# Performance work log

Hardware: AMD Instinct MI355X
Metric: run time of the kernel (lower is better)

Reference implementation:

```python
import jax, jax.numpy as jnp
import numpy as np
from jax import lax

B, T, N, H, NC = 2, 8, 512, 64, 10
NEG = -1e9
LN_EPS = 1e-5


def _gatv2(x, mask, Wl, Wr, att, b):
    # GATv2Conv (PyG semantics, eval mode): e_ij = att . leaky_relu(Wr x_i + Wl x_j),
    # softmax over source nodes j with self-loops, out_i = sum_j alpha_ij * (Wl x_j).
    # x: (B, N, Fin); mask: (N, N) bool adjacency incl. self-loops; att: (heads, C).
    heads, C = att.shape
    Bn, Nn, _ = x.shape
    xl = (x @ Wl).reshape(Bn, Nn, heads, C)  # source transform
    xr = (x @ Wr).reshape(Bn, Nn, heads, C)  # target transform
    s = jax.nn.leaky_relu(xr[:, :, None] + xl[:, None, :], 0.2)  # (B, Ni, Nj, h, C)
    e = jnp.einsum('bijhc,hc->bijh', s, att)
    e = jnp.where(mask[None, :, :, None], e, NEG)
    alpha = jax.nn.softmax(e, axis=2)  # softmax over neighbors j
    out = jnp.einsum('bijh,bjhc->bihc', alpha, xl)
    return out.reshape(Bn, Nn, heads * C) + b


def _gru_layer(x, Wih, Whh, bih, bhh):
    # torch nn.GRU single layer, batch_first; x: (B, T, Hin)
    h0 = jnp.zeros((x.shape[0], Whh.shape[0]), x.dtype)
    def step(h, xt):
        gi = xt @ Wih + bih
        gh = h @ Whh + bhh
        ir, iz, inn = jnp.split(gi, 3, axis=-1)
        hr, hz, hn = jnp.split(gh, 3, axis=-1)
        r = jax.nn.sigmoid(ir + hr)
        z = jax.nn.sigmoid(iz + hz)
        n = jnp.tanh(inn + r * hn)
        hnew = (1.0 - z) * n + z * h
        return hnew, hnew
    _, ys = lax.scan(step, h0, jnp.swapaxes(x, 0, 1))
    return jnp.swapaxes(ys, 0, 1)


def setup_inputs() -> dict:
    key = jax.random.key(0)
    ks = jax.random.split(key, 20)
    def rn(i, shape, s=0.1):
        return jax.random.normal(ks[i], shape, jnp.float32) * s
    x_seq = jax.random.normal(ks[0], (B, T, N, 1), jnp.float32)
    a = jax.random.uniform(ks[1], (N, N))
    up = jnp.triu((a > 0.95).astype(jnp.float32), 1)
    static_adj = up + up.T  # sparse symmetric 0/1 static graph
    dyn_W = jax.random.normal(ks[2], (N, N), jnp.float32)
    reg_lambda = jnp.array([0.05], jnp.float32)
    return {
        'x_seq': x_seq, 'static_adj': static_adj, 'dyn_W': dyn_W, 'reg_lambda': reg_lambda,
        'g1_Wl': rn(3, (1, H)), 'g1_Wr': rn(4, (1, H)), 'g1_att': rn(5, (4, H // 4)), 'g1_b': jnp.zeros(H),
        'g2_Wl': rn(6, (H, H)), 'g2_Wr': rn(7, (H, H)), 'g2_att': rn(8, (1, H)), 'g2_b': jnp.zeros(H),
        'gru_Wih0': rn(9, (H, 3 * H)), 'gru_Whh0': rn(10, (H, 3 * H)), 'gru_bih0': jnp.zeros(3 * H), 'gru_bhh0': jnp.zeros(3 * H),
        'gru_Wih1': rn(11, (H, 3 * H)), 'gru_Whh1': rn(12, (H, 3 * H)), 'gru_bih1': jnp.zeros(3 * H), 'gru_bhh1': jnp.zeros(3 * H),
        'attn_W': rn(13, (H, 1)), 'attn_b': jnp.zeros(1),
        'cls_W1': rn(14, (H, H)), 'cls_b1': jnp.zeros(H), 'ln_g': jnp.ones(H), 'ln_b': jnp.zeros(H),
        'cls_W2': rn(15, (H, NC)), 'cls_b2': jnp.zeros(NC),
    }


def reference(x_seq, static_adj, dyn_W, reg_lambda,
              g1_Wl, g1_Wr, g1_att, g1_b, g2_Wl, g2_Wr, g2_att, g2_b,
              gru_Wih0, gru_Whh0, gru_bih0, gru_bhh0,
              gru_Wih1, gru_Whh1, gru_bih1, gru_bhh1,
              attn_W, attn_b, cls_W1, cls_b1, ln_g, ln_b, cls_W2, cls_b2):
    Bn, Tn, Nn, _ = x_seq.shape
    lam = jnp.maximum(reg_lambda[0], 0.01)
    t = jnp.arange(Tn, dtype=x_seq.dtype)
    gts = jnp.exp(-lam * t)  # gating values per timestep
    dyn = jax.nn.relu(dyn_W + dyn_W.T)
    fused = gts[:, None, None] * static_adj + (1.0 - gts)[:, None, None] * dyn  # (T, N, N)
    masks = (fused > 0) | jnp.eye(Nn, dtype=bool)[None]  # edge set + self-loops

    def step(carry, inp):
        xt, mask = inp  # xt: (B, N, 1)
        h = jax.nn.elu(_gatv2(xt, mask, g1_Wl, g1_Wr, g1_att, g1_b))
        h = jax.nn.elu(_gatv2(h, mask, g2_Wl, g2_Wr, g2_att, g2_b))
        return carry, h.mean(axis=1)  # (B, H) graph readout

    _, reps = lax.scan(step, 0.0, (jnp.swapaxes(x_seq, 0, 1), masks))
    h_seq = jnp.swapaxes(reps, 0, 1)  # (B, T, H)

    gru_out = _gru_layer(h_seq, gru_Wih0, gru_Whh0, gru_bih0, gru_bhh0)
    gru_out = _gru_layer(gru_out, gru_Wih1, gru_Whh1, gru_bih1, gru_bhh1)

    att_scores = jax.nn.softmax((gru_out @ attn_W + attn_b)[..., 0], axis=1)  # (B, T)
    final = jnp.einsum('bt,bth->bh', att_scores, gru_out)

    z = final @ cls_W1 + cls_b1
    mu = jnp.mean(z, axis=-1, keepdims=True)
    var = jnp.var(z, axis=-1, keepdims=True)
    z = (z - mu) / jnp.sqrt(var + LN_EPS) * ln_g + ln_b
    z = jax.nn.gelu(z, approximate=False)
    logits = z @ cls_W2 + cls_b2
    return logits, gts, att_scores
```

## Files before the change

kernel.cpp:

```cpp
#include <hip/hip_runtime.h>
#include <math.h>

#define BB 2
#define TT 8
#define NN 512
#define HH 64
#define NC 10

typedef unsigned char uchar;

__device__ __forceinline__ float elu1(float v){ return v > 0.f ? v : expm1f(v); }
__device__ __forceinline__ float sigm(float v){ return 1.f/(1.f+expf(-v)); }

__global__ __launch_bounds__(256) void k_mask(
    const float* __restrict__ dW, const float* __restrict__ sadj,
    uchar* __restrict__ M0, uchar* __restrict__ M1,
    float* __restrict__ hseq,
    const float* __restrict__ att1, const float* __restrict__ Wr1,
    const float* __restrict__ Wl1, float* __restrict__ AB,
    const float* __restrict__ Whh0, const float* __restrict__ Wih1,
    const float* __restrict__ Whh1, float4* __restrict__ WT4)
{
    __shared__ float tr[64][65];
    int bx = blockIdx.x, by = blockIdx.y;
    int tid = threadIdx.x;
    if (blockIdx.z == 1){
        int idx = (by*8 + bx)*256 + tid;
        if (idx < 3*4096){
            int m = idx >> 12, r = idx & 4095;
            int gg = r >> 6, k = r & 63;
            const float* W = (m == 0) ? Whh0 : (m == 1) ? Wih1 : Whh1;
            float4 o;
            o.x = W[k*192 + gg];
            o.y = W[k*192 + 64 + gg];
            o.z = W[k*192 + 128 + gg];
            o.w = 0.f;
            WT4[(size_t)m*4096 + r] = o;
        }
        return;
    }
    int i0 = by*64, j0 = bx*64;
    #pragma unroll
    for (int q = 0; q < 4; ++q){
        int r = (tid >> 4) + 16*q, c4 = tid & 15;
        float4 v = *(const float4*)&dW[(size_t)(j0+r)*NN + i0 + 4*c4];
        tr[r][4*c4+0] = v.x; tr[r][4*c4+1] = v.y;
        tr[r][4*c4+2] = v.z; tr[r][4*c4+3] = v.w;
    }
    __syncthreads();
    #pragma unroll
    for (int q = 0; q < 4; ++q){
        int row = (tid >> 4) + 16*q, c4 = tid & 15;
        int i = i0 + row, j = j0 + 4*c4;
        float4 d  = *(const float4*)&dW[(size_t)i*NN + j];
        float4 sa = *(const float4*)&sadj[(size_t)i*NN + j];
        uchar4 m0, m1;
        float dd0 = d.x + tr[4*c4+0][row];
        float dd1 = d.y + tr[4*c4+1][row];
        float dd2 = d.z + tr[4*c4+2][row];
        float dd3 = d.w + tr[4*c4+3][row];
        m0.x = (sa.x > 0.f) || (i == j+0);
        m0.y = (sa.y > 0.f) || (i == j+1);
        m0.z = (sa.z > 0.f) || (i == j+2);
        m0.w = (sa.w > 0.f) || (i == j+3);
        m1.x = m0.x || (dd0 > 0.f);
        m1.y = m0.y || (dd1 > 0.f);
        m1.z = m0.z || (dd2 > 0.f);
        m1.w = m0.w || (dd3 > 0.f);
        *(uchar4*)&M0[(size_t)i*NN + j] = m0;
        *(uchar4*)&M1[(size_t)i*NN + j] = m1;
    }
    int flat = (by*8 + bx)*256 + tid;
    if (flat < BB*TT*HH) hseq[flat] = 0.f;
    if (bx == 0 && by == 0 && tid < 8){
        int h = tid & 3;
        const float* W = (tid < 4) ? Wr1 : Wl1;
        float s = 0.f;
        for (int c = 0; c < 16; ++c) s += att1[h*16+c]*W[h*16+c];
        AB[tid] = s;
    }
}

__global__ __launch_bounds__(256) void k_gat1f(
    const float* __restrict__ x_seq, const uchar* __restrict__ M0,
    const uchar* __restrict__ M1,
    const float* __restrict__ Wl, const float* __restrict__ Wr,
    const float* __restrict__ att, const float* __restrict__ bias,
    const float* __restrict__ AB,
    const float* __restrict__ Wl2, const float* __restrict__ Wr2,
    const float* __restrict__ att2,
    float* __restrict__ xl2, float* __restrict__ xr2,
    float* __restrict__ ui, float* __restrict__ vj)
{
    __shared__ float x_s[NN];
    __shared__ float S_s[4][4];
    __shared__ float h_s[4][HH];
    __shared__ float Wl2_s[64*64];
    __shared__ float Wr2_s[64*64];
    int bt = blockIdx.y; int t = bt % TT;
    int i0 = blockIdx.x * 4;
    int tid = threadIdx.x;
    int il = tid >> 6, jl = tid & 63;
    int i = i0 + il;
    const uchar* M = t ? M1 : M0;
    ((float2*)x_s)[tid] = ((const float2*)(x_seq + bt*NN))[tid];
    #pragma unroll
    for (int q = 0; q < 4; ++q){
        int idx = q*256 + tid;
        ((float4*)Wl2_s)[idx] = ((const float4*)Wl2)[idx];
        ((float4*)Wr2_s)[idx] = ((const float4*)Wr2)[idx];
    }
    __syncthreads();
    float xi = x_s[i];
    const uchar* Mrow = M + (size_t)i*NN;
    float xj[8], msk[8];
    #pragma unroll
    for (int jj = 0; jj < 8; ++jj){
        int j = jj*64 + jl;
        xj[jj] = x_s[j];
        msk[jj] = Mrow[j] ? 1.f : 0.f;
    }
    float sw[4] = {0,0,0,0}, swx[4] = {0,0,0,0};
    for (int h = 0; h < 4; ++h){
        float acc[8] = {0,0,0,0,0,0,0,0};
        #pragma unroll
        for (int c = 0; c < 16; ++c){
            int hc = h*16 + c;
            float wl = Wl[hc];
            float q  = 0.4f * att[hc];
            float pr = xi * Wr[hc];
            #pragma unroll
            for (int jj = 0; jj < 8; ++jj){
                float s = fmaf(xj[jj], wl, pr);
                acc[jj] = fmaf(q, fabsf(s), acc[jj]);
            }
        }
        float lin = 0.6f * xi * AB[h];
        float al6 = 0.6f * AB[4+h];
        #pragma unroll
        for (int jj = 0; jj < 8; ++jj){
            float e = acc[jj] + fmaf(al6, xj[jj], lin);
            float w = msk[jj] * __expf(e);
            sw[h] += w;
            swx[h] = fmaf(w, xj[jj], swx[h]);
        }
    }
    #pragma unroll
    for (int off = 32; off; off >>= 1){
        #pragma unroll
        for (int h = 0; h < 4; ++h){
            sw[h]  += __shfl_down(sw[h],  off);
            swx[h] += __shfl_down(swx[h], off);
        }
    }
    if (jl == 0){
        #pragma unroll
        for (int h = 0; h < 4; ++h) S_s[il][h] = swx[h] / sw[h];
    }
    __syncthreads();
    {
        int hc = tid & 63, row = tid >> 6;
        float v = S_s[row][hc >> 4] * Wl[hc] + bias[hc];
        h_s[row][hc] = elu1(v);
    }
    __syncthreads();
    {
        int c = tid & 63, row = tid >> 6;
        float al = 0.f, ar = 0.f;
        #pragma unroll 8
        for (int k = 0; k < 64; ++k){
            float hv = h_s[row][k];
            al = fmaf(hv, Wl2_s[k*64 + c], al);
            ar = fmaf(hv, Wr2_s[k*64 + c], ar);
        }
        size_t ridx = (size_t)(bt*NN + i0 + row);
        xl2[ridx*HH + c] = al;
        xr2[ridx*HH + c] = ar;
        float a2 = att2[c];
        float pu = a2 * ar, pv = a2 * al;
        #pragma unroll
        for (int off = 32; off; off >>= 1){
            pu += __shfl_down(pu, off);
            pv += __shfl_down(pv, off);
        }
        if (c == 0){ ui[ridx] = pu; vj[ridx] = pv; }
    }
}

__global__ __launch_bounds__(512) void k_gat2(
    const float* __restrict__ xl2, const float* __restrict__ xr2,
    const uchar* __restrict__ M0, const uchar* __restrict__ M1,
    const float* __restrict__ att, const float* __restrict__ ui,
    const float* __restrict__ vj, const float* __restrict__ bias,
    float* __restrict__ hseq)
{
    __shared__ float xl_s[256][68];
    __shared__ float wT_s[256][36];
    __shared__ float v_s[256];
    __shared__ float z_s[32];

    int bt = blockIdx.y, t = bt & 7;
    int i0 = blockIdx.x * 32;
    int base = bt * NN;
    int tid = threadIdx.x;
    const uchar* M = t ? M1 : M0;

    int ig = __builtin_amdgcn_readfirstlane(tid >> 6);
    int jg = tid & 63;
    int ln = jg;
    int ig2 = ln >> 3, cg2 = ln & 7;

    const float* xrp0 = xr2 + (size_t)(base + i0 + ig*4 + 0)*HH;
    const float* xrp1 = xr2 + (size_t)(base + i0 + ig*4 + 1)*HH;
    const float* xrp2 = xr2 + (size_t)(base + i0 + ig*4 + 2)*HH;
    const float* xrp3 = xr2 + (size_t)(base + i0 + ig*4 + 3)*HH;
    float u0 = 0.6f*ui[base + i0 + ig*4 + 0];
    float u1 = 0.6f*ui[base + i0 + ig*4 + 1];
    float u2 = 0.6f*ui[base + i0 + ig*4 + 2];
    float u3 = 0.6f*ui[base + i0 + ig*4 + 3];

    float zreg[4] = {0.f,0.f,0.f,0.f};
    float acc[4][8];
    #pragma unroll
    for (int a = 0; a < 4; ++a)
        #pragma unroll
        for (int r = 0; r < 8; ++r) acc[a][r] = 0.f;

    for (int tile = 0; tile < 2; ++tile){
        int j0 = tile * 256;
        __syncthreads();
        #pragma unroll
        for (int q = 0; q < 8; ++q){
            int idx = q*512 + tid;
            int row = idx >> 4, c4 = idx & 15;
            ((float4*)&xl_s[row][0])[c4] = ((const float4*)&xl2[(size_t)(base+j0+row)*HH])[c4];
        }
        if (tid < 256) v_s[tid] = vj[base + j0 + tid];
        __syncthreads();
        float e[4][4];
        #pragma unroll
        for (int jj = 0; jj < 4; ++jj){
            float vv = 0.6f * v_s[jj*64 + jg];
            e[0][jj] = u0 + vv; e[1][jj] = u1 + vv;
            e[2][jj] = u2 + vv; e[3][jj] = u3 + vv;
        }
        #pragma unroll 4
        for (int c4 = 0; c4 < 16; ++c4){
            float4 a4 = *(const float4*)&att[c4*4];
            float qk[4];
            qk[0] = 0.4f*a4.x; qk[1] = 0.4f*a4.y; qk[2] = 0.4f*a4.z; qk[3] = 0.4f*a4.w;
            float rr[4][4];
            *(float4*)rr[0] = *(const float4*)&xrp0[c4*4];
            *(float4*)rr[1] = *(const float4*)&xrp1[c4*4];
            *(float4*)rr[2] = *(const float4*)&xrp2[c4*4];
            *(float4*)rr[3] = *(const float4*)&xrp3[c4*4];
            float xlv[4][4];
            #pragma unroll
            for (int jj = 0; jj < 4; ++jj)
                *(float4*)xlv[jj] = ((const float4*)&xl_s[jj*64+jg][0])[c4];
            #pragma unroll
            for (int jj = 0; jj < 4; ++jj)
                #pragma unroll
                for (int k = 0; k < 4; ++k){
                    float xc = xlv[jj][k];
                    #pragma unroll
                    for (int ii = 0; ii < 4; ++ii)
                        e[ii][jj] = fmaf(qk[k], fabsf(rr[ii][k] + xc), e[ii][jj]);
                }
        }
        #pragma unroll
        for (int jj = 0; jj < 4; ++jj){
            int j = jj*64 + jg;
            const uchar* mp = &M[(size_t)(i0 + ig*4)*NN + j0 + j];
            float w0 = mp[0]      ? __expf(e[0][jj]) : 0.f;
            float w1 = mp[NN]     ? __expf(e[1][jj]) : 0.f;
            float w2 = mp[2*NN]   ? __expf(e[2][jj]) : 0.f;
            float w3 = mp[3*NN]   ? __expf(e[3][jj]) : 0.f;
            zreg[0] += w0; zreg[1] += w1; zreg[2] += w2; zreg[3] += w3;
            float4 wq; wq.x = w0; wq.y = w1; wq.z = w2; wq.w = w3;
            *(float4*)&wT_s[j][ig*4] = wq;
        }
        __syncthreads();
        #pragma unroll 4
        for (int jj = 0; jj < 32; ++jj){
            int j = ig*32 + jj;
            float w4[4], xa[8];
            *(float4*)w4      = *(const float4*)&wT_s[j][ig2*4];
            *(float4*)&xa[0]  = ((const float4*)&xl_s[j][0])[cg2*2+0];
            *(float4*)&xa[4]  = ((const float4*)&xl_s[j][0])[cg2*2+1];
            #pragma unroll
            for (int a = 0; a < 4; ++a)
                #pragma unroll
                for (int r = 0; r < 8; ++r)
                    acc[a][r] = fmaf(w4[a], xa[r], acc[a][r]);
        }
    }
    __syncthreads();
    #pragma unroll
    for (int off = 32; off; off >>= 1){
        #pragma unroll
        for (int ii = 0; ii < 4; ++ii) zreg[ii] += __shfl_down(zreg[ii], off);
    }
    if (jg == 0){
        #pragma unroll
        for (int ii = 0; ii < 4; ++ii) z_s[ig*4+ii] = zreg[ii];
    }
    float* scratch = &xl_s[0][0];
    if (ig > 0){
        #pragma unroll
        for (int a = 0; a < 4; ++a)
            #pragma unroll
            for (int r = 0; r < 8; ++r)
                scratch[(a*8+r)*448 + (ig-1)*64 + ln] = acc[a][r];
    }
    __syncthreads();
    if (ig == 0){
        float pm[8];
        #pragma unroll
        for (int r = 0; r < 8; ++r) pm[r] = 0.f;
        #pragma unroll
        for (int a = 0; a < 4; ++a){
            float rz = 1.f / z_s[ig2*4 + a];
            #pragma unroll
            for (int r = 0; r < 8; ++r){
                float s = acc[a][r];
                #pragma unroll
                for (int w = 0; w < 7; ++w)
                    s += scratch[(a*8+r)*448 + w*64 + ln];
                float h = elu1(s*rz + bias[cg2*8 + r]);
                pm[r] += h;
            }
        }
        #pragma unroll
        for (int off = 32; off >= 8; off >>= 1){
            #pragma unroll
            for (int r = 0; r < 8; ++r) pm[r] += __shfl_down(pm[r], off);
        }
        if (ig2 == 0){
            #pragma unroll
            for (int r = 0; r < 8; ++r)
                atomicAdd(&hseq[bt*HH + cg2*8 + r], pm[r] * (1.f/(float)NN));
        }
    }
}

__global__ __launch_bounds__(512) void k_gru2(
    const float* __restrict__ hseq, const float* __restrict__ Wih0,
    const float* __restrict__ bih0, const float4* __restrict__ WT4,
    const float* __restrict__ bhh0, const float* __restrict__ Wih1,
    const float* __restrict__ bih1, const float* __restrict__ bhh1,
    const float* __restrict__ lamp, const float* __restrict__ attn_W,
    const float* __restrict__ attn_b, const float* __restrict__ W1,
    const float* __restrict__ b1, const float* __restrict__ ln_g,
    const float* __restrict__ ln_b, const float* __restrict__ W2,
    const float* __restrict__ b2, float* __restrict__ out)
{
    __shared__ float gi_s[BB*TT*192];
    __shared__ float hs_s[BB*TT*HH];
    __shared__ float y_s[BB*TT*HH];
    __shared__ float h_lds[BB][HH];
    __shared__ float part_s[BB][2][3][HH];
    __shared__ float sc_s[BB][TT], at_s[BB][TT];
    __shared__ float fin_s[BB][HH], z_s[BB][HH], g_s[BB][HH];
    __shared__ float mu_s[BB], iv_s[BB];
    int tid = threadIdx.x;
    int wave = tid >> 6, lane = tid & 63;
    int gb = wave >> 1, half = wave & 1;
    bool gruw = (wave < 4);

    float4 Wreg[32];
    if (gruw){
        const float4* src = WT4 + (size_t)lane*64 + half*32;
        #pragma unroll
        for (int kk = 0; kk < 32; ++kk) Wreg[kk] = src[kk];
    }
    for (int v = tid; v < BB*TT*HH; v += 512) hs_s[v] = hseq[v];
    if (tid < BB*HH) h_lds[tid >> 6][tid & 63] = 0.f;
    __syncthreads();
    #pragma unroll
    for (int o = 0; o < 6; ++o){
        int idx = o*512 + tid;
        int b = idx / 192, g = idx % 192;
        float a = bih0[g];
        const float* hr = &hs_s[b*HH];
        #pragma unroll 8
        for (int k = 0; k < HH; ++k) a = fmaf(hr[k], Wih0[k*192 + g], a);
        gi_s[idx] = a;
    }
    __syncthreads();
    {
        float bhr = 0.f, bhz = 0.f, bhn = 0.f;
        if (gruw && half == 0){ bhr = bhh0[lane]; bhz = bhh0[64+lane]; bhn = bhh0[128+lane]; }
        for (int t = 0; t < TT; ++t){
            if (gruw){
                float hh[32];
                #pragma unroll
                for (int q = 0; q < 8; ++q)
                    *(float4*)&hh[q*4] = *(const float4*)&h_lds[gb][half*32 + q*4];
                float ar0=0,ar1=0,az0=0,az1=0,an0=0,an1=0;
                #pragma unroll
                for (int kk = 0; kk < 32; kk += 2){
                    ar0 = fmaf(Wreg[kk].x,   hh[kk],   ar0);
                    az0 = fmaf(Wreg[kk].y,   hh[kk],   az0);
                    an0 = fmaf(Wreg[kk].z,   hh[kk],   an0);
                    ar1 = fmaf(Wreg[kk+1].x, hh[kk+1], ar1);
                    az1 = fmaf(Wreg[kk+1].y, hh[kk+1], az1);
                    an1 = fmaf(Wreg[kk+1].z, hh[kk+1], an1);
                }
                part_s[gb][half][0][lane] = ar0 + ar1;
                part_s[gb][half][1][lane] = az0 + az1;
                part_s[gb][half][2][lane] = an0 + an1;
            }
            __syncthreads();
            if (gruw && half == 0){
                float ghr = part_s[gb][0][0][lane] + part_s[gb][1][0][lane] + bhr;
                float ghz = part_s[gb][0][1][lane] + part_s[gb][1][1][lane] + bhz;
                float ghn = part_s[gb][0][2][lane] + part_s[gb][1][2][lane] + bhn;
                const float* gi = &gi_s[(gb*TT + t)*192];
                float r = sigm(gi[lane] + ghr);
                float z = sigm(gi[64+lane] + ghz);
                float n = tanhf(gi[128+lane] + r*ghn);
                float hn = (1.f - z)*n + z*h_lds[gb][lane];
                h_lds[gb][lane] = hn;
                y_s[(gb*TT + t)*HH + lane] = hn;
            }
            __syncthreads();
        }
    }
    if (gruw){
        const float4* src = WT4 + 2*4096 + (size_t)lane*64 + half*32;
        #pragma unroll
        for (int kk = 0; kk < 32; ++kk) Wreg[kk] = src[kk];
    }
    #pragma unroll
    for (int o = 0; o < 6; ++o){
        int idx = o*512 + tid;
        int b = idx / 192, g = idx % 192;
        float a = bih1[g];
        const float* yr = &y_s[b*HH];
        #pragma unroll 8
        for (int k = 0; k < HH; ++k) a = fmaf(yr[k], Wih1[k*192 + g], a);
        gi_s[idx] = a;
    }
    if (tid < BB*HH) h_lds[tid >> 6][tid & 63] = 0.f;
    __syncthreads();
    {
        float bhr = 0.f, bhz = 0.f, bhn = 0.f;
        if (gruw && half == 0){ bhr = bhh1[lane]; bhz = bhh1[64+lane]; bhn = bhh1[128+lane]; }
        for (int t = 0; t < TT; ++t){
            if (gruw){
                float hh[32];
                #pragma unroll
                for (int q = 0; q < 8; ++q)
                    *(float4*)&hh[q*4] = *(const float4*)&h_lds[gb][half*32 + q*4];
                float ar0=0,ar1=0,az0=0,az1=0,an0=0,an1=0;
                #pragma unroll
                for (int kk = 0; kk < 32; kk += 2){
                    ar0 = fmaf(Wreg[kk].x,   hh[kk],   ar0);
                    az0 = fmaf(Wreg[kk].y,   hh[kk],   az0);
                    an0 = fmaf(Wreg[kk].z,   hh[kk],   an0);
                    ar1 = fmaf(Wreg[kk+1].x, hh[kk+1], ar1);
                    az1 = fmaf(Wreg[kk+1].y, hh[kk+1], az1);
                    an1 = fmaf(Wreg[kk+1].z, hh[kk+1], an1);
                }
                part_s[gb][half][0][lane] = ar0 + ar1;
                part_s[gb][half][1][lane] = az0 + az1;
                part_s[gb][half][2][lane] = an0 + an1;
            }
            __syncthreads();
            if (gruw && half == 0){
                float ghr = part_s[gb][0][0][lane] + part_s[gb][1][0][lane] + bhr;
                float ghz = part_s[gb][0][1][lane] + part_s[gb][1][1][lane] + bhz;
                float ghn = part_s[gb][0][2][lane] + part_s[gb][1][2][lane] + bhn;
                const float* gi = &gi_s[(gb*TT + t)*192];
                float r = sigm(gi[lane] + ghr);
                float z = sigm(gi[64+lane] + ghz);
                float n = tanhf(gi[128+lane] + r*ghn);
                float hn = (1.f - z)*n + z*h_lds[gb][lane];
                h_lds[gb][lane] = hn;
                y_s[(gb*TT + t)*HH + lane] = hn;
            }
            __syncthreads();
        }
    }
    float lam = fmaxf(lamp[0], 0.01f);
    if (tid < TT) out[BB*NC + tid] = expf(-lam*(float)tid);
    if (tid < BB*TT){
        int bb = tid >> 3, t = tid & 7;
        float s = attn_b[0];
        const float* r = &y_s[(bb*TT+t)*HH];
        for (int h = 0; h < HH; ++h) s += r[h]*attn_W[h];
        sc_s[bb][t] = s;
    }
    __syncthreads();
    if (tid < BB){
        float mx = -INFINITY;
        for (int t = 0; t < TT; ++t) mx = fmaxf(mx, sc_s[tid][t]);
        float se = 0.f;
        for (int t = 0; t < TT; ++t){ float w = expf(sc_s[tid][t]-mx); at_s[tid][t] = w; se += w; }
        for (int t = 0; t < TT; ++t){
            at_s[tid][t] /= se;
            out[BB*NC + TT + tid*TT + t] = at_s[tid][t];
        }
    }
    __syncthreads();
    if (tid < BB*HH){
        int bb = tid >> 6, h = tid & 63;
        float a = 0.f;
        for (int t = 0; t < TT; ++t) a += at_s[bb][t]*y_s[(bb*TT+t)*HH + h];
        fin_s[bb][h] = a;
    }
    __syncthreads();
    if (tid < BB*HH){
        int bb = tid >> 6, h = tid & 63;
        float a = b1[h];
        for (int k = 0; k < HH; ++k) a += fin_s[bb][k]*W1[k*HH+h];
        z_s[bb][h] = a;
    }
    __syncthreads();
    if (tid < BB){
        float mu = 0.f;
        for (int h = 0; h < HH; ++h) mu += z_s[tid][h];
        mu *= (1.f/HH);
        float v = 0.f;
        for (int h = 0; h < HH; ++h){ float d = z_s[tid][h]-mu; v += d*d; }
        v *= (1.f/HH);
        mu_s[tid] = mu; iv_s[tid] = 1.f/sqrtf(v + 1e-5f);
    }
    __syncthreads();
    if (tid < BB*HH){
        int bb = tid >> 6, h = tid & 63;
        float zn = (z_s[bb][h]-mu_s[bb])*iv_s[bb]*ln_g[h] + ln_b[h];
        g_s[bb][h] = 0.5f*zn*(1.f + erff(zn*0.70710678118654752f));
    }
    __syncthreads();
    if (tid < BB*NC){
        int bb = tid / NC, c = tid % NC;
        float a = b2[c];
        for (int k = 0; k < HH; ++k) a += g_s[bb][k]*W2[k*NC+c];
        out[bb*NC + c] = a;
    }
}

extern "C" void kernel_launch(void* const* d_in, const int* in_sizes, int n_in,
                              void* d_out, int out_size, void* d_ws, size_t ws_size,
                              hipStream_t stream)
{
    const float* x_seq = (const float*)d_in[0];
    const float* sadj  = (const float*)d_in[1];
    const float* dynW  = (const float*)d_in[2];
    const float* lamp  = (const float*)d_in[3];
    const float* g1_Wl = (const float*)d_in[4];
    const float* g1_Wr = (const float*)d_in[5];
    const float* g1_att= (const float*)d_in[6];
    const float* g1_b  = (const float*)d_in[7];
    const float* g2_Wl = (const float*)d_in[8];
    const float* g2_Wr = (const float*)d_in[9];
    const float* g2_att= (const float*)d_in[10];
    const float* g2_b  = (const float*)d_in[11];
    const float* Wih0  = (const float*)d_in[12];
    const float* Whh0  = (const float*)d_in[13];
    const float* bih0  = (const float*)d_in[14];
    const float* bhh0  = (const float*)d_in[15];
    const float* Wih1  = (const float*)d_in[16];
    const float* Whh1  = (const float*)d_in[17];
    const float* bih1  = (const float*)d_in[18];
    const float* bhh1  = (const float*)d_in[19];
    const float* attnW = (const float*)d_in[20];
    const float* attnb = (const float*)d_in[21];
    const float* W1    = (const float*)d_in[22];
    const float* b1    = (const float*)d_in[23];
    const float* lng   = (const float*)d_in[24];
    const float* lnb   = (const float*)d_in[25];
    const float* W2    = (const float*)d_in[26];
    const float* b2    = (const float*)d_in[27];
    float* out = (float*)d_out;

    const int RWS = BB*TT*NN*HH;
    uchar* M0 = (uchar*)d_ws;
    uchar* M1 = M0 + (size_t)NN*NN;
    float* fb = (float*)(M1 + (size_t)NN*NN);
    float* AB   = fb;
    float* ui   = AB   + 16;
    float* vj   = ui   + BB*TT*NN;
    float* xl2  = vj   + BB*TT*NN;
    float* xr2  = xl2  + RWS;
    float* hseq = xr2  + RWS;
    float4* WT4 = (float4*)(hseq + BB*TT*HH);

    k_mask <<<dim3(8,8,2), 256, 0, stream>>>(dynW, sadj, M0, M1, hseq, g1_att, g1_Wr, g1_Wl, AB,
                                             Whh0, Wih1, Whh1, WT4);
    k_gat1f<<<dim3(NN/4, BB*TT), 256, 0, stream>>>(x_seq, M0, M1, g1_Wl, g1_Wr, g1_att, g1_b, AB,
                                                   g2_Wl, g2_Wr, g2_att, xl2, xr2, ui, vj);
    k_gat2 <<<dim3(NN/32, BB*TT), 512, 0, stream>>>(xl2, xr2, M0, M1, g2_att, ui, vj, g2_b, hseq);
    k_gru2 <<<1, 512, 0, stream>>>(hseq, Wih0, bih0, WT4, bhh0, Wih1, bih1, bhh1,
                                   lamp, attnW, attnb, W1, b1, lng, lnb, W2, b2, out);
}
```

Measured before the change: 223.2 us.

## Fuse all four kernels into one cooperative persistent kernel with grid syncs

Replaces the four separate launches (mask, GAT layer 1, GAT layer 2, GRU/classifier) with a single cooperative kernel of 256 blocks that separates the phases with grid.sync, using a shared-memory union across phases. Work is remapped onto fixed blocks: GAT1 blocks loop over several row tiles, and the weight-transposition work for the GRU is redistributed. The aim is to remove launch gaps and per-kernel ramp-up between phases. In exchange it adds grid-wide barriers and fixes the block count, which may reduce occupancy and parallelism in the heavy GAT phases. The union's LDS footprint is also set by the largest phase.

```diff
diff --git a/kernel.cpp b/kernel.cpp
--- a/kernel.cpp
+++ b/kernel.cpp
@@ -1,5 +1,8 @@
 #include <hip/hip_runtime.h>
+#include <hip/hip_cooperative_groups.h>
 #include <math.h>
+
+namespace cg = cooperative_groups;
 
 #define BB 2
 #define TT 8
@@ -12,533 +15,521 @@
 __device__ __forceinline__ float elu1(float v){ return v > 0.f ? v : expm1f(v); }
 __device__ __forceinline__ float sigm(float v){ return 1.f/(1.f+expf(-v)); }
 
-__global__ __launch_bounds__(256) void k_mask(
-    const float* __restrict__ dW, const float* __restrict__ sadj,
-    uchar* __restrict__ M0, uchar* __restrict__ M1,
-    float* __restrict__ hseq,
-    const float* __restrict__ att1, const float* __restrict__ Wr1,
-    const float* __restrict__ Wl1, float* __restrict__ AB,
-    const float* __restrict__ Whh0, const float* __restrict__ Wih1,
-    const float* __restrict__ Whh1, float4* __restrict__ WT4)
+struct Prm {
+    const float *x_seq, *sadj, *dynW, *lamp;
+    const float *g1_Wl, *g1_Wr, *g1_att, *g1_b;
+    const float *g2_Wl, *g2_Wr, *g2_att, *g2_b;
+    const float *Wih0, *Whh0, *bih0, *bhh0;
+    const float *Wih1, *Whh1, *bih1, *bhh1;
+    const float *attnW, *attnb, *W1, *b1, *lng, *lnb, *W2, *b2;
+    uchar *M0, *M1;
+    float *AB, *ui, *vj, *xl2, *xr2, *hseq;
+    float4 *WT4;
+    float *out;
+};
+
+union __align__(16) SharedU {
+    struct { float tr[64][65]; } p0;
+    struct { float x_s[NN]; float Wl2[64*64]; float Wr2[64*64];
+             float S_s[8][4]; float h_s[8][HH]; } p1;
+    struct { float xl_s[256][68]; float wT_s[256][36];
+             float v_s[256]; float z_s[32]; } p2;
+    struct { float gi[BB*TT*192]; float hs[BB*TT*HH]; float y[BB*TT*HH];
+             float h_lds[BB][HH]; float part[BB][2][3][HH];
+             float sc[BB][TT]; float at[BB][TT];
+             float fin[BB][HH]; float z[BB][HH]; float g[BB][HH];
+             float mu[BB]; float iv[BB]; } p3;
+};
+
+__global__ __launch_bounds__(512) void k_fused(Prm p)
 {
-    __shared__ float tr[64][65];
-    int bx = blockIdx.x, by = blockIdx.y;
-    int tid = threadIdx.x;
-    if (blockIdx.z == 1){
-        int idx = (by*8 + bx)*256 + tid;
-        if (idx < 3*4096){
-            int m = idx >> 12, r = idx & 4095;
-            int gg = r >> 6, k = r & 63;
-            const float* W = (m == 0) ? Whh0 : (m == 1) ? Wih1 : Whh1;
-            float4 o;
-            o.x = W[k*192 + gg];
-            o.y = W[k*192 + 64 + gg];
-            o.z = W[k*192 + 128 + gg];
-            o.w = 0.f;
-            WT4[(size_t)m*4096 + r] = o;
-        }
-        return;
-    }
-    int i0 = by*64, j0 = bx*64;
-    #pragma unroll
-    for (int q = 0; q < 4; ++q){
-        int r = (tid >> 4) + 16*q, c4 = tid & 15;
-        float4 v = *(const float4*)&dW[(size_t)(j0+r)*NN + i0 + 4*c4];
-        tr[r][4*c4+0] = v.x; tr[r][4*c4+1] = v.y;
-        tr[r][4*c4+2] = v.z; tr[r][4*c4+3] = v.w;
-    }
-    __syncthreads();
-    #pragma unroll
-    for (int q = 0; q < 4; ++q){
-        int row = (tid >> 4) + 16*q, c4 = tid & 15;
-        int i = i0 + row, j = j0 + 4*c4;
-        float4 d  = *(const float4*)&dW[(size_t)i*NN + j];
-        float4 sa = *(const float4*)&sadj[(size_t)i*NN + j];
-        uchar4 m0, m1;
-        float dd0 = d.x + tr[4*c4+0][row];
-        float dd1 = d.y + tr[4*c4+1][row];
-        float dd2 = d.z + tr[4*c4+2][row];
-        float dd3 = d.w + tr[4*c4+3][row];
-        m0.x = (sa.x > 0.f) || (i == j+0);
-        m0.y = (sa.y > 0.f) || (i == j+1);
-        m0.z = (sa.z > 0.f) || (i == j+2);
-        m0.w = (sa.w > 0.f) || (i == j+3);
-        m1.x = m0.x || (dd0 > 0.f);
-        m1.y = m0.y || (dd1 > 0.f);
-        m1.z = m0.z || (dd2 > 0.f);
-        m1.w = m0.w || (dd3 > 0.f);
-        *(uchar4*)&M0[(size_t)i*NN + j] = m0;
-        *(uchar4*)&M1[(size_t)i*NN + j] = m1;
-    }
-    int flat = (by*8 + bx)*256 + tid;
-    if (flat < BB*TT*HH) hseq[flat] = 0.f;
-    if (bx == 0 && by == 0 && tid < 8){
-        int h = tid & 3;
-        const float* W = (tid < 4) ? Wr1 : Wl1;
-        float s = 0.f;
-        for (int c = 0; c < 16; ++c) s += att1[h*16+c]*W[h*16+c];
-        AB[tid] = s;
-    }
-}
-
-__global__ __launch_bounds__(256) void k_gat1f(
-    const float* __restrict__ x_seq, const uchar* __restrict__ M0,
-    const uchar* __restrict__ M1,
-    const float* __restrict__ Wl, const float* __restrict__ Wr,
-    const float* __restrict__ att, const float* __restrict__ bias,
-    const float* __restrict__ AB,
-    const float* __restrict__ Wl2, const float* __restrict__ Wr2,
-    const float* __restrict__ att2,
-    float* __restrict__ xl2, float* __restrict__ xr2,
-    float* __restrict__ ui, float* __restrict__ vj)
-{
-    __shared__ float x_s[NN];
-    __shared__ float S_s[4][4];
-    __shared__ float h_s[4][HH];
-    __shared__ float Wl2_s[64*64];
-    __shared__ float Wr2_s[64*64];
-    int bt = blockIdx.y; int t = bt % TT;
-    int i0 = blockIdx.x * 4;
-    int tid = threadIdx.x;
-    int il = tid >> 6, jl = tid & 63;
-    int i = i0 + il;
-    const uchar* M = t ? M1 : M0;
-    ((float2*)x_s)[tid] = ((const float2*)(x_seq + bt*NN))[tid];
-    #pragma unroll
-    for (int q = 0; q < 4; ++q){
-        int idx = q*256 + tid;
-        ((float4*)Wl2_s)[idx] = ((const float4*)Wl2)[idx];
-        ((float4*)Wr2_s)[idx] = ((const float4*)Wr2)[idx];
-    }
-    __syncthreads();
-    float xi = x_s[i];
-    const uchar* Mrow = M + (size_t)i*NN;
-    float xj[8], msk[8];
-    #pragma unroll
-    for (int jj = 0; jj < 8; ++jj){
-        int j = jj*64 + jl;
-        xj[jj] = x_s[j];
-        msk[jj] = Mrow[j] ? 1.f : 0.f;
-    }
-    float sw[4] = {0,0,0,0}, swx[4] = {0,0,0,0};
-    for (int h = 0; h < 4; ++h){
-        float acc[8] = {0,0,0,0,0,0,0,0};
-        #pragma unroll
-        for (int c = 0; c < 16; ++c){
-            int hc = h*16 + c;
-            float wl = Wl[hc];
-            float q  = 0.4f * att[hc];
-            float pr = xi * Wr[hc];
-            #pragma unroll
-            for (int jj = 0; jj < 8; ++jj){
-                float s = fmaf(xj[jj], wl, pr);
-                acc[jj] = fmaf(q, fabsf(s), acc[jj]);
-            }
-        }
-        float lin = 0.6f * xi * AB[h];
-        float al6 = 0.6f * AB[4+h];
-        #pragma unroll
-        for (int jj = 0; jj < 8; ++jj){
-            float e = acc[jj] + fmaf(al6, xj[jj], lin);
-            float w = msk[jj] * __expf(e);
-            sw[h] += w;
-            swx[h] = fmaf(w, xj[jj], swx[h]);
-        }
-    }
-    #pragma unroll
-    for (int off = 32; off; off >>= 1){
-        #pragma unroll
-        for (int h = 0; h < 4; ++h){
-            sw[h]  += __shfl_down(sw[h],  off);
-            swx[h] += __shfl_down(swx[h], off);
-        }
-    }
-    if (jl == 0){
-        #pragma unroll
-        for (int h = 0; h < 4; ++h) S_s[il][h] = swx[h] / sw[h];
-    }
-    __syncthreads();
-    {
-        int hc = tid & 63, row = tid >> 6;
-        float v = S_s[row][hc >> 4] * Wl[hc] + bias[hc];
-        h_s[row][hc] = elu1(v);
-    }
-    __syncthreads();
-    {
-        int c = tid & 63, row = tid >> 6;
-        float al = 0.f, ar = 0.f;
-        #pragma unroll 8
-        for (int k = 0; k < 64; ++k){
-            float hv = h_s[row][k];
-            al = fmaf(hv, Wl2_s[k*64 + c], al);
-            ar = fmaf(hv, Wr2_s[k*64 + c], ar);
-        }
-        size_t ridx = (size_t)(bt*NN + i0 + row);
-        xl2[ridx*HH + c] = al;
-        xr2[ridx*HH + c] = ar;
-        float a2 = att2[c];
-        float pu = a2 * ar, pv = a2 * al;
-        #pragma unroll
-        for (int off = 32; off; off >>= 1){
-            pu += __shfl_down(pu, off);
-            pv += __shfl_down(pv, off);
-        }
-        if (c == 0){ ui[ridx] = pu; vj[ridx] = pv; }
-    }
-}
-
-__global__ __launch_bounds__(512) void k_gat2(
-    const float* __restrict__ xl2, const float* __restrict__ xr2,
-    const uchar* __restrict__ M0, const uchar* __restrict__ M1,
-    const float* __restrict__ att, const float* __restrict__ ui,
-    const float* __restrict__ vj, const float* __restrict__ bias,
-    float* __restrict__ hseq)
-{
-    __shared__ float xl_s[256][68];
-    __shared__ float wT_s[256][36];
-    __shared__ float v_s[256];
-    __shared__ float z_s[32];
-
-    int bt = blockIdx.y, t = bt & 7;
-    int i0 = blockIdx.x * 32;
-    int base = bt * NN;
-    int tid = threadIdx.x;
-    const uchar* M = t ? M1 : M0;
-
-    int ig = __builtin_amdgcn_readfirstlane(tid >> 6);
-    int jg = tid & 63;
-    int ln = jg;
-    int ig2 = ln >> 3, cg2 = ln & 7;
-
-    const float* xrp0 = xr2 + (size_t)(base + i0 + ig*4 + 0)*HH;
-    const float* xrp1 = xr2 + (size_t)(base + i0 + ig*4 + 1)*HH;
-    const float* xrp2 = xr2 + (size_t)(base + i0 + ig*4 + 2)*HH;
-    const float* xrp3 = xr2 + (size_t)(base + i0 + ig*4 + 3)*HH;
-    float u0 = 0.6f*ui[base + i0 + ig*4 + 0];
-    float u1 = 0.6f*ui[base + i0 + ig*4 + 1];
-    float u2 = 0.6f*ui[base + i0 + ig*4 + 2];
-    float u3 = 0.6f*ui[base + i0 + ig*4 + 3];
-
-    float zreg[4] = {0.f,0.f,0.f,0.f};
-    float acc[4][8];
-    #pragma unroll
-    for (int a = 0; a < 4; ++a)
-        #pragma unroll
-        for (int r = 0; r < 8; ++r) acc[a][r] = 0.f;
-
-    for (int tile = 0; tile < 2; ++tile){
-        int j0 = tile * 256;
-        __syncthreads();
-        #pragma unroll
-        for (int q = 0; q < 8; ++q){
+    __shared__ SharedU sh;
+    cg::grid_group grid = cg::this_grid();
+    int bid = blockIdx.x, tid = threadIdx.x;
+
+    if (bid < 64){
+        int by = bid >> 3, bx = bid & 7;
+        int i0 = by*64, j0 = bx*64;
+        #pragma unroll
+        for (int q = 0; q < 2; ++q){
+            int idx = q*512 + tid;
+            int r = idx >> 4, c4 = idx & 15;
+            float4 v = *(const float4*)&p.dynW[(size_t)(j0+r)*NN + i0 + 4*c4];
+            sh.p0.tr[r][4*c4+0] = v.x; sh.p0.tr[r][4*c4+1] = v.y;
+            sh.p0.tr[r][4*c4+2] = v.z; sh.p0.tr[r][4*c4+3] = v.w;
+        }
+        __syncthreads();
+        #pragma unroll
+        for (int q = 0; q < 2; ++q){
             int idx = q*512 + tid;
             int row = idx >> 4, c4 = idx & 15;
-            ((float4*)&xl_s[row][0])[c4] = ((const float4*)&xl2[(size_t)(base+j0+row)*HH])[c4];
-        }
-        if (tid < 256) v_s[tid] = vj[base + j0 + tid];
-        __syncthreads();
-        float e[4][4];
-        #pragma unroll
-        for (int jj = 0; jj < 4; ++jj){
-            float vv = 0.6f * v_s[jj*64 + jg];
-            e[0][jj] = u0 + vv; e[1][jj] = u1 + vv;
-            e[2][jj] = u2 + vv; e[3][jj] = u3 + vv;
-        }
-        #pragma unroll 4
-        for (int c4 = 0; c4 < 16; ++c4){
-            float4 a4 = *(const float4*)&att[c4*4];
-            float qk[4];
-            qk[0] = 0.4f*a4.x; qk[1] = 0.4f*a4.y; qk[2] = 0.4f*a4.z; qk[3] = 0.4f*a4.w;
-            float rr[4][4];
-            *(float4*)rr[0] = *(const float4*)&xrp0[c4*4];
-            *(float4*)rr[1] = *(const float4*)&xrp1[c4*4];
-            *(float4*)rr[2] = *(const float4*)&xrp2[c4*4];
-            *(float4*)rr[3] = *(const float4*)&xrp3[c4*4];
-            float xlv[4][4];
-            #pragma unroll
-            for (int jj = 0; jj < 4; ++jj)
-                *(float4*)xlv[jj] = ((const float4*)&xl_s[jj*64+jg][0])[c4];
-            #pragma unroll
-            for (int jj = 0; jj < 4; ++jj)
-                #pragma unroll
-                for (int k = 0; k < 4; ++k){
-                    float xc = xlv[jj][k];
-                    #pragma unroll
-                    for (int ii = 0; ii < 4; ++ii)
-                        e[ii][jj] = fmaf(qk[k], fabsf(rr[ii][k] + xc), e[ii][jj]);
-                }
-        }
-        #pragma unroll
-        for (int jj = 0; jj < 4; ++jj){
-            int j = jj*64 + jg;
-            const uchar* mp = &M[(size_t)(i0 + ig*4)*NN + j0 + j];
-            float w0 = mp[0]      ? __expf(e[0][jj]) : 0.f;
-            float w1 = mp[NN]     ? __expf(e[1][jj]) : 0.f;
-            float w2 = mp[2*NN]   ? __expf(e[2][jj]) : 0.f;
-            float w3 = mp[3*NN]   ? __expf(e[3][jj]) : 0.f;
-            zreg[0] += w0; zreg[1] += w1; zreg[2] += w2; zreg[3] += w3;
-            float4 wq; wq.x = w0; wq.y = w1; wq.z = w2; wq.w = w3;
-            *(float4*)&wT_s[j][ig*4] = wq;
-        }
-        __syncthreads();
-        #pragma unroll 4
-        for (int jj = 0; jj < 32; ++jj){
-            int j = ig*32 + jj;
-            float w4[4], xa[8];
-            *(float4*)w4      = *(const float4*)&wT_s[j][ig2*4];
-            *(float4*)&xa[0]  = ((const float4*)&xl_s[j][0])[cg2*2+0];
-            *(float4*)&xa[4]  = ((const float4*)&xl_s[j][0])[cg2*2+1];
+            int i = i0 + row, j = j0 + 4*c4;
+            float4 d  = *(const float4*)&p.dynW[(size_t)i*NN + j];
+            float4 sa = *(const float4*)&p.sadj[(size_t)i*NN + j];
+            uchar4 m0, m1;
+            float dd0 = d.x + sh.p0.tr[4*c4+0][row];
+            float dd1 = d.y + sh.p0.tr[4*c4+1][row];
+            float dd2 = d.z + sh.p0.tr[4*c4+2][row];
+            float dd3 = d.w + sh.p0.tr[4*c4+3][row];
+            m0.x = (sa.x > 0.f) || (i == j+0);
+            m0.y = (sa.y > 0.f) || (i == j+1);
+            m0.z = (sa.z > 0.f) || (i == j+2);
+            m0.w = (sa.w > 0.f) || (i == j+3);
+            m1.x = m0.x || (dd0 > 0.f);
+            m1.y = m0.y || (dd1 > 0.f);
+            m1.z = m0.z || (dd2 > 0.f);
+            m1.w = m0.w || (dd3 > 0.f);
+            *(uchar4*)&p.M0[(size_t)i*NN + j] = m0;
+            *(uchar4*)&p.M1[(size_t)i*NN + j] = m1;
+        }
+    } else if (bid < 80){
+        int idx = (bid - 64)*512 + tid;
+        int m = idx >> 12, r = idx & 4095;
+        int k = r >> 6, gg = r & 63;
+        const float* W = m ? p.Whh1 : p.Whh0;
+        float4 o;
+        o.x = W[k*192 + gg];
+        o.y = W[k*192 + 64 + gg];
+        o.z = W[k*192 + 128 + gg];
+        o.w = 0.f;
+        p.WT4[(size_t)m*4096 + r] = o;
+    } else if (bid == 80){
+        p.hseq[tid] = 0.f;
+        p.hseq[512 + tid] = 0.f;
+    } else if (bid == 81){
+        if (tid < 8){
+            int h = tid & 3;
+            const float* W = (tid < 4) ? p.g1_Wr : p.g1_Wl;
+            float s = 0.f;
+            for (int c = 0; c < 16; ++c) s += p.g1_att[h*16+c]*W[h*16+c];
+            p.AB[tid] = s;
+        }
+    }
+    grid.sync();
+
+    {
+        #pragma unroll
+        for (int q = 0; q < 2; ++q){
+            int idx = q*512 + tid;
+            ((float4*)sh.p1.Wl2)[idx] = ((const float4*)p.g2_Wl)[idx];
+            ((float4*)sh.p1.Wr2)[idx] = ((const float4*)p.g2_Wr)[idx];
+        }
+        int w = tid >> 6, jl = tid & 63;
+        for (int s = 0; s < 4; ++s){
+            int vb = bid*4 + s;
+            int bt = vb >> 6, it = vb & 63;
+            int i0v = it*8;
+            int t = bt & 7;
+            const uchar* M = t ? p.M1 : p.M0;
+            __syncthreads();
+            sh.p1.x_s[tid] = p.x_seq[bt*NN + tid];
+            __syncthreads();
+            int i = i0v + w;
+            float xi = sh.p1.x_s[i];
+            const uchar* Mrow = M + (size_t)i*NN;
+            float xj[8], msk[8];
+            #pragma unroll
+            for (int jj = 0; jj < 8; ++jj){
+                int j = jj*64 + jl;
+                xj[jj] = sh.p1.x_s[j];
+                msk[jj] = Mrow[j] ? 1.f : 0.f;
+            }
+            float sw[4] = {0,0,0,0}, swx[4] = {0,0,0,0};
+            for (int h = 0; h < 4; ++h){
+                float acc[8] = {0,0,0,0,0,0,0,0};
+                #pragma unroll
+                for (int c = 0; c < 16; ++c){
+                    int hc = h*16 + c;
+                    float wl = p.g1_Wl[hc];
+                    float q  = 0.4f * p.g1_att[hc];
+                    float pr = xi * p.g1_Wr[hc];
+                    #pragma unroll
+                    for (int jj = 0; jj < 8; ++jj){
+                        float sv = fmaf(xj[jj], wl, pr);
+                        acc[jj] = fmaf(q, fabsf(sv), acc[jj]);
+                    }
+                }
+                float lin = 0.6f * xi * p.AB[h];
+                float al6 = 0.6f * p.AB[4+h];
+                #pragma unroll
+                for (int jj = 0; jj < 8; ++jj){
+                    float e = acc[jj] + fmaf(al6, xj[jj], lin);
+                    float ww = msk[jj] * __expf(e);
+                    sw[h] += ww;
+                    swx[h] = fmaf(ww, xj[jj], swx[h]);
+                }
+            }
+            #pragma unroll
+            for (int off = 32; off; off >>= 1){
+                #pragma unroll
+                for (int h = 0; h < 4; ++h){
+                    sw[h]  += __shfl_down(sw[h],  off);
+                    swx[h] += __shfl_down(swx[h], off);
+                }
+            }
+            if (jl == 0){
+                #pragma unroll
+                for (int h = 0; h < 4; ++h) sh.p1.S_s[w][h] = swx[h] / sw[h];
+            }
+            __syncthreads();
+            {
+                int hc = tid & 63, row = tid >> 6;
+                float v = sh.p1.S_s[row][hc >> 4] * p.g1_Wl[hc] + p.g1_b[hc];
+                sh.p1.h_s[row][hc] = elu1(v);
+            }
+            __syncthreads();
+            {
+                int c = tid & 63, row = tid >> 6;
+                float al = 0.f, ar = 0.f;
+                #pragma unroll 8
+                for (int k = 0; k < 64; ++k){
+                    float hv = sh.p1.h_s[row][k];
+                    al = fmaf(hv, sh.p1.Wl2[k*64 + c], al);
+                    ar = fmaf(hv, sh.p1.Wr2[k*64 + c], ar);
+                }
+                size_t ridx = (size_t)(bt*NN + i0v + row);
+                p.xl2[ridx*HH + c] = al;
+                p.xr2[ridx*HH + c] = ar;
+                float a2 = p.g2_att[c];
+                float pu = a2 * ar, pv = a2 * al;
+                #pragma unroll
+                for (int off = 32; off; off >>= 1){
+                    pu += __shfl_down(pu, off);
+                    pv += __shfl_down(pv, off);
+                }
+                if (c == 0){ p.ui[ridx] = pu; p.vj[ridx] = pv; }
+            }
+        }
+    }
+    grid.sync();
+
+    {
+        int bt = bid >> 4, t = bt & 7;
+        int i0 = (bid & 15) * 32;
+        int base = bt * NN;
+        const uchar* M = t ? p.M1 : p.M0;
+
+        int ig = __builtin_amdgcn_readfirstlane(tid >> 6);
+        int jg = tid & 63;
+        int ln = jg;
+        int ig2 = ln >> 3, cg2 = ln & 7;
+
+        const float* xrp0 = p.xr2 + (size_t)(base + i0 + ig*4 + 0)*HH;
+        const float* xrp1 = p.xr2 + (size_t)(base + i0 + ig*4 + 1)*HH;
+        const float* xrp2 = p.xr2 + (size_t)(base + i0 + ig*4 + 2)*HH;
+        const float* xrp3 = p.xr2 + (size_t)(base + i0 + ig*4 + 3)*HH;
+        float u0 = 0.6f*p.ui[base + i0 + ig*4 + 0];
+        float u1 = 0.6f*p.ui[base + i0 + ig*4 + 1];
+        float u2 = 0.6f*p.ui[base + i0 + ig*4 + 2];
+        float u3 = 0.6f*p.ui[base + i0 + ig*4 + 3];
+
+        float zreg[4] = {0.f,0.f,0.f,0.f};
+        float acc[4][8];
+        #pragma unroll
+        for (int a = 0; a < 4; ++a)
+            #pragma unroll
+            for (int r = 0; r < 8; ++r) acc[a][r] = 0.f;
+
+        for (int tile = 0; tile < 2; ++tile){
+            int j0 = tile * 256;
+            __syncthreads();
+            #pragma unroll
+            for (int q = 0; q < 8; ++q){
+                int idx = q*512 + tid;
+                int row = idx >> 4, c4 = idx & 15;
+                ((float4*)&sh.p2.xl_s[row][0])[c4] =
+                    ((const float4*)&p.xl2[(size_t)(base+j0+row)*HH])[c4];
+            }
+            if (tid < 256) sh.p2.v_s[tid] = p.vj[base + j0 + tid];
+            __syncthreads();
+            float e[4][4];
+            #pragma unroll
+            for (int jj = 0; jj < 4; ++jj){
+                float vv = 0.6f * sh.p2.v_s[jj*64 + jg];
+                e[0][jj] = u0 + vv; e[1][jj] = u1 + vv;
+                e[2][jj] = u2 + vv; e[3][jj] = u3 + vv;
+            }
+            #pragma unroll 4
+            for (int c4 = 0; c4 < 16; ++c4){
+                float4 a4 = *(const float4*)&p.g2_att[c4*4];
+                float qk[4];
+                qk[0] = 0.4f*a4.x; qk[1] = 0.4f*a4.y; qk[2] = 0.4f*a4.z; qk[3] = 0.4f*a4.w;
+                float rr[4][4];
+                *(float4*)rr[0] = *(const float4*)&xrp0[c4*4];
+                *(float4*)rr[1] = *(const float4*)&xrp1[c4*4];
+                *(float4*)rr[2] = *(const float4*)&xrp2[c4*4];
+                *(float4*)rr[3] = *(const float4*)&xrp3[c4*4];
+                float xlv[4][4];
+                #pragma unroll
+                for (int jj = 0; jj < 4; ++jj)
+                    *(float4*)xlv[jj] = ((const float4*)&sh.p2.xl_s[jj*64+jg][0])[c4];
+                #pragma unroll
+                for (int jj = 0; jj < 4; ++jj)
+                    #pragma unroll
+                    for (int k = 0; k < 4; ++k){
+                        float xc = xlv[jj][k];
+                        #pragma unroll
+                        for (int ii = 0; ii < 4; ++ii)
+                            e[ii][jj] = fmaf(qk[k], fabsf(rr[ii][k] + xc), e[ii][jj]);
+                    }
+            }
+            #pragma unroll
+            for (int jj = 0; jj < 4; ++jj){
+                int j = jj*64 + jg;
+                const uchar* mp = &M[(size_t)(i0 + ig*4)*NN + j0 + j];
+                float w0 = mp[0]      ? __expf(e[0][jj]) : 0.f;
+                float w1 = mp[NN]     ? __expf(e[1][jj]) : 0.f;
+                float w2 = mp[2*NN]   ? __expf(e[2][jj]) : 0.f;
+                float w3 = mp[3*NN]   ? __expf(e[3][jj]) : 0.f;
+                zreg[0] += w0; zreg[1] += w1; zreg[2] += w2; zreg[3] += w3;
+                float4 wq; wq.x = w0; wq.y = w1; wq.z = w2; wq.w = w3;
+                *(float4*)&sh.p2.wT_s[j][ig*4] = wq;
+            }
+            __syncthreads();
+            #pragma unroll 4
+            for (int jj = 0; jj < 32; ++jj){
+                int j = ig*32 + jj;
+                float w4[4], xa[8];
+                *(float4*)w4      = *(const float4*)&sh.p2.wT_s[j][ig2*4];
+                *(float4*)&xa[0]  = ((const float4*)&sh.p2.xl_s[j][0])[cg2*2+0];
+                *(float4*)&xa[4]  = ((const float4*)&sh.p2.xl_s[j][0])[cg2*2+1];
+                #pragma unroll
+                for (int a = 0; a < 4; ++a)
+                    #pragma unroll
+                    for (int r = 0; r < 8; ++r)
+                        acc[a][r] = fmaf(w4[a], xa[r], acc[a][r]);
+            }
+        }
+        __syncthreads();
+        #pragma unroll
+        for (int off = 32; off; off >>= 1){
+            #pragma unroll
+            for (int ii = 0; ii < 4; ++ii) zreg[ii] += __shfl_down(zreg[ii], off);
+        }
+        if (jg == 0){
+            #pragma unroll
+            for (int ii = 0; ii < 4; ++ii) sh.p2.z_s[ig*4+ii] = zreg[ii];
+        }
+        float* scratch = &sh.p2.xl_s[0][0];
+        if (ig > 0){
             #pragma unroll
             for (int a = 0; a < 4; ++a)
                 #pragma unroll
                 for (int r = 0; r < 8; ++r)
-                    acc[a][r] = fmaf(w4[a], xa[r], acc[a][r]);
+                    scratch[(a*8+r)*448 + (ig-1)*64 + ln] = acc[a][r];
+        }
+        __syncthreads();
+        if (ig == 0){
+            float pm[8];
+            #pragma unroll
+            for (int r = 0; r < 8; ++r) pm[r] = 0.f;
+            #pragma unroll
+            for (int a = 0; a < 4; ++a){
+                float rz = 1.f / sh.p2.z_s[ig2*4 + a];
+                #pragma unroll
+                for (int r = 0; r < 8; ++r){
+                    float s = acc[a][r];
+                    #pragma unroll
+                    for (int w = 0; w < 7; ++w)
+                        s += scratch[(a*8+r)*448 + w*64 + ln];
+                    float h = elu1(s*rz + p.g2_b[cg2*8 + r]);
+                    pm[r] += h;
+                }
+            }
+            #pragma unroll
+            for (int off = 32; off >= 8; off >>= 1){
+                #pragma unroll
+                for (int r = 0; r < 8; ++r) pm[r] += __shfl_down(pm[r], off);
+            }
+            if (ig2 == 0){
+                #pragma unroll
+                for (int r = 0; r < 8; ++r)
+                    atomicAdd(&p.hseq[bt*HH + cg2*8 + r], pm[r] * (1.f/(float)NN));
+            }
         }
     }
-    __syncthreads();
-    #pragma unroll
-    for (int off = 32; off; off >>= 1){
-        #pragma unroll
-        for (int ii = 0; ii < 4; ++ii) zreg[ii] += __shfl_down(zreg[ii], off);
-    }
-    if (jg == 0){
-        #pragma unroll
-        for (int ii = 0; ii < 4; ++ii) z_s[ig*4+ii] = zreg[ii];
-    }
-    float* scratch = &xl_s[0][0];
-    if (ig > 0){
-        #pragma unroll
-        for (int a = 0; a < 4; ++a)
-            #pragma unroll
-            for (int r = 0; r < 8; ++r)
-                scratch[(a*8+r)*448 + (ig-1)*64 + ln] = acc[a][r];
-    }
-    __syncthreads();
-    if (ig == 0){
-        float pm[8];
-        #pragma unroll
-        for (int r = 0; r < 8; ++r) pm[r] = 0.f;
-        #pragma unroll
-        for (int a = 0; a < 4; ++a){
-            float rz = 1.f / z_s[ig2*4 + a];
-            #pragma unroll
-            for (int r = 0; r < 8; ++r){
-                float s = acc[a][r];
-                #pragma unroll
-                for (int w = 0; w < 7; ++w)
-                    s += scratch[(a*8+r)*448 + w*64 + ln];
-                float h = elu1(s*rz + bias[cg2*8 + r]);
-                pm[r] += h;
-            }
-        }
-        #pragma unroll
-        for (int off = 32; off >= 8; off >>= 1){
-            #pragma unroll
-            for (int r = 0; r < 8; ++r) pm[r] += __shfl_down(pm[r], off);
-        }
-        if (ig2 == 0){
-            #pragma unroll
-            for (int r = 0; r < 8; ++r)
-                atomicAdd(&hseq[bt*HH + cg2*8 + r], pm[r] * (1.f/(float)NN));
-        }
-    }
-}
-
-__global__ __launch_bounds__(512) void k_gru2(
-    const float* __restrict__ hseq, const float* __restrict__ Wih0,
-    const float* __restrict__ bih0, const float4* __restrict__ WT4,
-    const float* __restrict__ bhh0, const float* __restrict__ Wih1,
-    const float* __restrict__ bih1, const float* __restrict__ bhh1,
-    const float* __restrict__ lamp, const float* __restrict__ attn_W,
-    const float* __restrict__ attn_b, const float* __restrict__ W1,
-    const float* __restrict__ b1, const float* __restrict__ ln_g,
-    const float* __restrict__ ln_b, const float* __restrict__ W2,
-    const float* __restrict__ b2, float* __restrict__ out)
-{
-    __shared__ float gi_s[BB*TT*192];
-    __shared__ float hs_s[BB*TT*HH];
-    __shared__ float y_s[BB*TT*HH];
-    __shared__ float h_lds[BB][HH];
-    __shared__ float part_s[BB][2][3][HH];
-    __shared__ float sc_s[BB][TT], at_s[BB][TT];
-    __shared__ float fin_s[BB][HH], z_s[BB][HH], g_s[BB][HH];
-    __shared__ float mu_s[BB], iv_s[BB];
-    int tid = threadIdx.x;
-    int wave = tid >> 6, lane = tid & 63;
-    int gb = wave >> 1, half = wave & 1;
-    bool gruw = (wave < 4);
-
-    float4 Wreg[32];
-    if (gruw){
-        const float4* src = WT4 + (size_t)lane*64 + half*32;
-        #pragma unroll
-        for (int kk = 0; kk < 32; ++kk) Wreg[kk] = src[kk];
-    }
-    for (int v = tid; v < BB*TT*HH; v += 512) hs_s[v] = hseq[v];
-    if (tid < BB*HH) h_lds[tid >> 6][tid & 63] = 0.f;
-    __syncthreads();
-    #pragma unroll
-    for (int o = 0; o < 6; ++o){
-        int idx = o*512 + tid;
-        int b = idx / 192, g = idx % 192;
-        float a = bih0[g];
-        const float* hr = &hs_s[b*HH];
-        #pragma unroll 8
-        for (int k = 0; k < HH; ++k) a = fmaf(hr[k], Wih0[k*192 + g], a);
-        gi_s[idx] = a;
-    }
-    __syncthreads();
+    grid.sync();
+
+    if (bid != 0) return;
     {
-        float bhr = 0.f, bhz = 0.f, bhn = 0.f;
-        if (gruw && half == 0){ bhr = bhh0[lane]; bhz = bhh0[64+lane]; bhn = bhh0[128+lane]; }
-        for (int t = 0; t < TT; ++t){
-            if (gruw){
-                float hh[32];
-                #pragma unroll
-                for (int q = 0; q < 8; ++q)
-                    *(float4*)&hh[q*4] = *(const float4*)&h_lds[gb][half*32 + q*4];
-                float ar0=0,ar1=0,az0=0,az1=0,an0=0,an1=0;
-                #pragma unroll
-                for (int kk = 0; kk < 32; kk += 2){
-                    ar0 = fmaf(Wreg[kk].x,   hh[kk],   ar0);
-                    az0 = fmaf(Wreg[kk].y,   hh[kk],   az0);
-                    an0 = fmaf(Wreg[kk].z,   hh[kk],   an0);
-                    ar1 = fmaf(Wreg[kk+1].x, hh[kk+1], ar1);
-                    az1 = fmaf(Wreg[kk+1].y, hh[kk+1], az1);
-                    an1 = fmaf(Wreg[kk+1].z, hh[kk+1], an1);
-                }
-                part_s[gb][half][0][lane] = ar0 + ar1;
-                part_s[gb][half][1][lane] = az0 + az1;
-                part_s[gb][half][2][lane] = an0 + an1;
-            }
-            __syncthreads();
-            if (gruw && half == 0){
-                float ghr = part_s[gb][0][0][lane] + part_s[gb][1][0][lane] + bhr;
-                float ghz = part_s[gb][0][1][lane] + part_s[gb][1][1][lane] + bhz;
-                float ghn = part_s[gb][0][2][lane] + part_s[gb][1][2][lane] + bhn;
-                const float* gi = &gi_s[(gb*TT + t)*192];
-                float r = sigm(gi[lane] + ghr);
-                float z = sigm(gi[64+lane] + ghz);
-                float n = tanhf(gi[128+lane] + r*ghn);
-                float hn = (1.f - z)*n + z*h_lds[gb][lane];
-                h_lds[gb][lane] = hn;
-                y_s[(gb*TT + t)*HH + lane] = hn;
-            }
-            __syncthreads();
-        }
-    }
-    if (gruw){
-        const float4* src = WT4 + 2*4096 + (size_t)lane*64 + half*32;
-        #pragma unroll
-        for (int kk = 0; kk < 32; ++kk) Wreg[kk] = src[kk];
-    }
-    #pragma unroll
-    for (int o = 0; o < 6; ++o){
-        int idx = o*512 + tid;
-        int b = idx / 192, g = idx % 192;
-        float a = bih1[g];
-        const float* yr = &y_s[b*HH];
-        #pragma unroll 8
-        for (int k = 0; k < HH; ++k) a = fmaf(yr[k], Wih1[k*192 + g], a);
-        gi_s[idx] = a;
-    }
-    if (tid < BB*HH) h_lds[tid >> 6][tid & 63] = 0.f;
-    __syncthreads();
-    {
-        float bhr = 0.f, bhz = 0.f, bhn = 0.f;
-        if (gruw && half == 0){ bhr = bhh1[lane]; bhz = bhh1[64+lane]; bhn = bhh1[128+lane]; }
-        for (int t = 0; t < TT; ++t){
-            if (gruw){
-                float hh[32];
-                #pragma unroll
-                for (int q = 0; q < 8; ++q)
-                    *(float4*)&hh[q*4] = *(const float4*)&h_lds[gb][half*32 + q*4];
-                float ar0=0,ar1=0,az0=0,az1=0,an0=0,an1=0;
-                #pragma unroll
-                for (int kk = 0; kk < 32; kk += 2){
-                    ar0 = fmaf(Wreg[kk].x,   hh[kk],   ar0);
-                    az0 = fmaf(Wreg[kk].y,   hh[kk],   az0);
-                    an0 = fmaf(Wreg[kk].z,   hh[kk],   an0);
-                    ar1 = fmaf(Wreg[kk+1].x, hh[kk+1], ar1);
-                    az1 = fmaf(Wreg[kk+1].y, hh[kk+1], az1);
-                    an1 = fmaf(Wreg[kk+1].z, hh[kk+1], an1);
-                }
-                part_s[gb][half][0][lane] = ar0 + ar1;
-                part_s[gb][half][1][lane] = az0 + az1;
-                part_s[gb][half][2][lane] = an0 + an1;
-            }
-            __syncthreads();
-            if (gruw && half == 0){
-                float ghr = part_s[gb][0][0][lane] + part_s[gb][1][0][lane] + bhr;
-                float ghz = part_s[gb][0][1][lane] + part_s[gb][1][1][lane] + bhz;
-                float ghn = part_s[gb][0][2][lane] + part_s[gb][1][2][lane] + bhn;
-                const float* gi = &gi_s[(gb*TT + t)*192];
-                float r = sigm(gi[lane] + ghr);
-                float z = sigm(gi[64+lane] + ghz);
-                float n = tanhf(gi[128+lane] + r*ghn);
-                float hn = (1.f - z)*n + z*h_lds[gb][lane];
-                h_lds[gb][lane] = hn;
-                y_s[(gb*TT + t)*HH + lane] = hn;
-            }
-            __syncthreads();
-        }
-    }
-    float lam = fmaxf(lamp[0], 0.01f);
-    if (tid < TT) out[BB*NC + tid] = expf(-lam*(float)tid);
-    if (tid < BB*TT){
-        int bb = tid >> 3, t = tid & 7;
-        float s = attn_b[0];
-        const float* r = &y_s[(bb*TT+t)*HH];
-        for (int h = 0; h < HH; ++h) s += r[h]*attn_W[h];
-        sc_s[bb][t] = s;
-    }
-    __syncthreads();
-    if (tid < BB){
-        float mx = -INFINITY;
-        for (int t = 0; t < TT; ++t) mx = fmaxf(mx, sc_s[tid][t]);
-        float se = 0.f;
-        for (int t = 0; t < TT; ++t){ float w = expf(sc_s[tid][t]-mx); at_s[tid][t] = w; se += w; }
-        for (int t = 0; t < TT; ++t){
-            at_s[tid][t] /= se;
-            out[BB*NC + TT + tid*TT + t] = at_s[tid][t];
-        }
-    }
-    __syncthreads();
-    if (tid < BB*HH){
-        int bb = tid >> 6, h = tid & 63;
-        float a = 0.f;
-        for (int t = 0; t < TT; ++t) a += at_s[bb][t]*y_s[(bb*TT+t)*HH + h];
-        fin_s[bb][h] = a;
-    }
-    __syncthreads();
-    if (tid < BB*HH){
-        int bb = tid >> 6, h = tid & 63;
-        float a = b1[h];
-        for (int k = 0; k < HH; ++k) a += fin_s[bb][k]*W1[k*HH+h];
-        z_s[bb][h] = a;
-    }
-    __syncthreads();
-    if (tid < BB){
-        float mu = 0.f;
-        for (int h = 0; h < HH; ++h) mu += z_s[tid][h];
-        mu *= (1.f/HH);
-        float v = 0.f;
-        for (int h = 0; h < HH; ++h){ float d = z_s[tid][h]-mu; v += d*d; }
-        v *= (1.f/HH);
-        mu_s[tid] = mu; iv_s[tid] = 1.f/sqrtf(v + 1e-5f);
-    }
-    __syncthreads();
-    if (tid < BB*HH){
-        int bb = tid >> 6, h = tid & 63;
-        float zn = (z_s[bb][h]-mu_s[bb])*iv_s[bb]*ln_g[h] + ln_b[h];
-        g_s[bb][h] = 0.5f*zn*(1.f + erff(zn*0.70710678118654752f));
-    }
-    __syncthreads();
-    if (tid < BB*NC){
-        int bb = tid / NC, c = tid % NC;
-        float a = b2[c];
-        for (int k = 0; k < HH; ++k) a += g_s[bb][k]*W2[k*NC+c];
-        out[bb*NC + c] = a;
+        int wave = tid >> 6, lane = tid & 63;
+        int gb = wave >> 1, half = wave & 1;
+        bool gruw = (wave < 4);
+
+        float4 Wreg[32];
+        if (gruw){
+            const float4* src = p.WT4;
+            #pragma unroll
+            for (int kk = 0; kk < 32; ++kk)
+                Wreg[kk] = src[(size_t)(half*32 + kk)*64 + lane];
+        }
+        for (int v = tid; v < BB*TT*HH; v += 512) sh.p3.hs[v] = p.hseq[v];
+        if (tid < BB*HH) sh.p3.h_lds[tid >> 6][tid & 63] = 0.f;
+        __syncthreads();
+        #pragma unroll
+        for (int o = 0; o < 6; ++o){
+            int idx = o*512 + tid;
+            int b = idx / 192, g = idx % 192;
+            float a = p.bih0[g];
+            const float* hr = &sh.p3.hs[b*HH];
+            #pragma unroll 8
+            for (int k = 0; k < HH; ++k) a = fmaf(hr[k], p.Wih0[k*192 + g], a);
+            sh.p3.gi[idx] = a;
+        }
+        __syncthreads();
+        {
+            float bhr = 0.f, bhz = 0.f, bhn = 0.f;
+            if (gruw && half == 0){ bhr = p.bhh0[lane]; bhz = p.bhh0[64+lane]; bhn = p.bhh0[128+lane]; }
+            for (int t = 0; t < TT; ++t){
+                if (gruw){
+                    float hh[32];
+                    #pragma unroll
+                    for (int q = 0; q < 8; ++q)
+                        *(float4*)&hh[q*4] = *(const float4*)&sh.p3.h_lds[gb][half*32 + q*4];
+                    float ar0=0,ar1=0,az0=0,az1=0,an0=0,an1=0;
+                    #pragma unroll
+                    for (int kk = 0; kk < 32; kk += 2){
+                        ar0 = fmaf(Wreg[kk].x,   hh[kk],   ar0);
+                        az0 = fmaf(Wreg[kk].y,   hh[kk],   az0);
+                        an0 = fmaf(Wreg[kk].z,   hh[kk],   an0);
+                        ar1 = fmaf(Wreg[kk+1].x, hh[kk+1], ar1);
+                        az1 = fmaf(Wreg[kk+1].y, hh[kk+1], az1);
+                        an1 = fmaf(Wreg[kk+1].z, hh[kk+1], an1);
+                    }
+                    sh.p3.part[gb][half][0][lane] = ar0 + ar1;
+                    sh.p3.part[gb][half][1][lane] = az0 + az1;
+                    sh.p3.part[gb][half][2][lane] = an0 + an1;
+                }
+                __syncthreads();
+                if (gruw && half == 0){
+                    float ghr = sh.p3.part[gb][0][0][lane] + sh.p3.part[gb][1][0][lane] + bhr;
+                    float ghz = sh.p3.part[gb][0][1][lane] + sh.p3.part[gb][1][1][lane] + bhz;
+                    float ghn = sh.p3.part[gb][0][2][lane] + sh.p3.part[gb][1][2][lane] + bhn;
+                    const float* gi = &sh.p3.gi[(gb*TT + t)*192];
+                    float r = sigm(gi[lane] + ghr);
+                    float z = sigm(gi[64+lane] + ghz);
+                    float n = tanhf(gi[128+lane] + r*ghn);
+                    float hn = (1.f - z)*n + z*sh.p3.h_lds[gb][lane];
+                    sh.p3.h_lds[gb][lane] = hn;
+                    sh.p3.y[(gb*TT + t)*HH + lane] = hn;
+                }
+                __syncthreads();
+            }
+        }
+        if (gruw){
+            const float4* src = p.WT4 + 4096;
+            #pragma unroll
+            for (int kk = 0; kk < 32; ++kk)
+                Wreg[kk] = src[(size_t)(half*32 + kk)*64 + lane];
+        }
+        #pragma unroll
+        for (int o = 0; o < 6; ++o){
+            int idx = o*512 + tid;
+            int b = idx / 192, g = idx % 192;
+            float a = p.bih1[g];
+            const float* yr = &sh.p3.y[b*HH];
+            #pragma unroll 8
+            for (int k = 0; k < HH; ++k) a = fmaf(yr[k], p.Wih1[k*192 + g], a);
+            sh.p3.gi[idx] = a;
+        }
+        if (tid < BB*HH) sh.p3.h_lds[tid >> 6][tid & 63] = 0.f;
+        __syncthreads();
+        {
+            float bhr = 0.f, bhz = 0.f, bhn = 0.f;
+            if (gruw && half == 0){ bhr = p.bhh1[lane]; bhz = p.bhh1[64+lane]; bhn = p.bhh1[128+lane]; }
+            for (int t = 0; t < TT; ++t){
+                if (gruw){
+                    float hh[32];
+                    #pragma unroll
+                    for (int q = 0; q < 8; ++q)
+                        *(float4*)&hh[q*4] = *(const float4*)&sh.p3.h_lds[gb][half*32 + q*4];
+                    float ar0=0,ar1=0,az0=0,az1=0,an0=0,an1=0;
+                    #pragma unroll
+                    for (int kk = 0; kk < 32; kk += 2){
+                        ar0 = fmaf(Wreg[kk].x,   hh[kk],   ar0);
+                        az0 = fmaf(Wreg[kk].y,   hh[kk],   az0);
+                        an0 = fmaf(Wreg[kk].z,   hh[kk],   an0);
+                        ar1 = fmaf(Wreg[kk+1].x, hh[kk+1], ar1);
+                        az1 = fmaf(Wreg[kk+1].y, hh[kk+1], az1);
+                        an1 = fmaf(Wreg[kk+1].z, hh[kk+1], an1);
+                    }
+                    sh.p3.part[gb][half][0][lane] = ar0 + ar1;
+                    sh.p3.part[gb][half][1][lane] = az0 + az1;
+                    sh.p3.part[gb][half][2][lane] = an0 + an1;
+                }
+                __syncthreads();
+                if (gruw && half == 0){
+                    float ghr = sh.p3.part[gb][0][0][lane] + sh.p3.part[gb][1][0][lane] + bhr;
+                    float ghz = sh.p3.part[gb][0][1][lane] + sh.p3.part[gb][1][1][lane] + bhz;
+                    float ghn = sh.p3.part[gb][0][2][lane] + sh.p3.part[gb][1][2][lane] + bhn;
+                    const float* gi = &sh.p3.gi[(gb*TT + t)*192];
+                    float r = sigm(gi[lane] + ghr);
+                    float z = sigm(gi[64+lane] + ghz);
+                    float n = tanhf(gi[128+lane] + r*ghn);
+                    float hn = (1.f - z)*n + z*sh.p3.h_lds[gb][lane];
+                    sh.p3.h_lds[gb][lane] = hn;
+                    sh.p3.y[(gb*TT + t)*HH + lane] = hn;
+                }
+                __syncthreads();
+            }
+        }
+        float lam = fmaxf(p.lamp[0], 0.01f);
+        if (tid < TT) p.out[BB*NC + tid] = expf(-lam*(float)tid);
+        if (tid < BB*TT){
+            int bb = tid >> 3, t = tid & 7;
+            float s = p.attnb[0];
+            const float* r = &sh.p3.y[(bb*TT+t)*HH];
+            for (int h = 0; h < HH; ++h) s += r[h]*p.attnW[h];
+            sh.p3.sc[bb][t] = s;
+        }
+        __syncthreads();
+        if (tid < BB){
+            float mx = -INFINITY;
+            for (int t = 0; t < TT; ++t) mx = fmaxf(mx, sh.p3.sc[tid][t]);
+            float se = 0.f;
+            for (int t = 0; t < TT; ++t){ float w = expf(sh.p3.sc[tid][t]-mx); sh.p3.at[tid][t] = w; se += w; }
+            for (int t = 0; t < TT; ++t){
+                sh.p3.at[tid][t] /= se;
+                p.out[BB*NC + TT + tid*TT + t] = sh.p3.at[tid][t];
+            }
+        }
+        __syncthreads();
+        if (tid < BB*HH){
+            int bb = tid >> 6, h = tid & 63;
+            float a = 0.f;
+            for (int t = 0; t < TT; ++t) a += sh.p3.at[bb][t]*sh.p3.y[(bb*TT+t)*HH + h];
+            sh.p3.fin[bb][h] = a;
+        }
+        __syncthreads();
+        if (tid < BB*HH){
+            int bb = tid >> 6, h = tid & 63;
+            float a = p.b1[h];
+            for (int k = 0; k < HH; ++k) a += sh.p3.fin[bb][k]*p.W1[k*HH+h];
+            sh.p3.z[bb][h] = a;
+        }
+        __syncthreads();
+        if (tid < BB){
+            float mu = 0.f;
+            for (int h = 0; h < HH; ++h) mu += sh.p3.z[tid][h];
+            mu *= (1.f/HH);
+            float v = 0.f;
+            for (int h = 0; h < HH; ++h){ float d = sh.p3.z[tid][h]-mu; v += d*d; }
+            v *= (1.f/HH);
+            sh.p3.mu[tid] = mu; sh.p3.iv[tid] = 1.f/sqrtf(v + 1e-5f);
+        }
+        __syncthreads();
+        if (tid < BB*HH){
+            int bb = tid >> 6, h = tid & 63;
+            float zn = (sh.p3.z[bb][h]-sh.p3.mu[bb])*sh.p3.iv[bb]*p.lng[h] + p.lnb[h];
+            sh.p3.g[bb][h] = 0.5f*zn*(1.f + erff(zn*0.70710678118654752f));
+        }
+        __syncthreads();
+        if (tid < BB*NC){
+            int bb = tid / NC, c = tid % NC;
+            float a = p.b2[c];
+            for (int k = 0; k < HH; ++k) a += sh.p3.g[bb][k]*p.W2[k*NC+c];
+            p.out[bb*NC + c] = a;
+        }
     }
 }
 
@@ -546,53 +537,50 @@
                               void* d_out, int out_size, void* d_ws, size_t ws_size,
                               hipStream_t stream)
 {
-    const float* x_seq = (const float*)d_in[0];
-    const float* sadj  = (const float*)d_in[1];
-    const float* dynW  = (const float*)d_in[2];
-    const float* lamp  = (const float*)d_in[3];
-    const float* g1_Wl = (const float*)d_in[4];
-    const float* g1_Wr = (const float*)d_in[5];
-    const float* g1_att= (const float*)d_in[6];
-    const float* g1_b  = (const float*)d_in[7];
-    const float* g2_Wl = (const float*)d_in[8];
-    const float* g2_Wr = (const float*)d_in[9];
-    const float* g2_att= (const float*)d_in[10];
-    const float* g2_b  = (const float*)d_in[11];
-    const float* Wih0  = (const float*)d_in[12];
-    const float* Whh0  = (const float*)d_in[13];
-    const float* bih0  = (const float*)d_in[14];
-    const float* bhh0  = (const float*)d_in[15];
-    const float* Wih1  = (const float*)d_in[16];
-    const float* Whh1  = (const float*)d_in[17];
-    const float* bih1  = (const float*)d_in[18];
-    const float* bhh1  = (const float*)d_in[19];
-    const float* attnW = (const float*)d_in[20];
-    const float* attnb = (const float*)d_in[21];
-    const float* W1    = (const float*)d_in[22];
-    const float* b1    = (const float*)d_in[23];
-    const float* lng   = (const float*)d_in[24];
-    const float* lnb   = (const float*)d_in[25];
-    const float* W2    = (const float*)d_in[26];
-    const float* b2    = (const float*)d_in[27];
-    float* out = (float*)d_out;
+    Prm p;
+    p.x_seq = (const float*)d_in[0];
+    p.sadj  = (const float*)d_in[1];
+    p.dynW  = (const float*)d_in[2];
+    p.lamp  = (const float*)d_in[3];
+    p.g1_Wl = (const float*)d_in[4];
+    p.g1_Wr = (const float*)d_in[5];
+    p.g1_att= (const float*)d_in[6];
+    p.g1_b  = (const float*)d_in[7];
+    p.g2_Wl = (const float*)d_in[8];
+    p.g2_Wr = (const float*)d_in[9];
+    p.g2_att= (const float*)d_in[10];
+    p.g2_b  = (const float*)d_in[11];
+    p.Wih0  = (const float*)d_in[12];
+    p.Whh0  = (const float*)d_in[13];
+    p.bih0  = (const float*)d_in[14];
+    p.bhh0  = (const float*)d_in[15];
+    p.Wih1  = (const float*)d_in[16];
+    p.Whh1  = (const float*)d_in[17];
+    p.bih1  = (const float*)d_in[18];
+    p.bhh1  = (const float*)d_in[19];
+    p.attnW = (const float*)d_in[20];
+    p.attnb = (const float*)d_in[21];
+    p.W1    = (const float*)d_in[22];
+    p.b1    = (const float*)d_in[23];
+    p.lng   = (const float*)d_in[24];
+    p.lnb   = (const float*)d_in[25];
+    p.W2    = (const float*)d_in[26];
+    p.b2    = (const float*)d_in[27];
+    p.out   = (float*)d_out;
 
     const int RWS = BB*TT*NN*HH;
-    uchar* M0 = (uchar*)d_ws;
-    uchar* M1 = M0 + (size_t)NN*NN;
-    float* fb = (float*)(M1 + (size_t)NN*NN);
-    float* AB   = fb;
-    float* ui   = AB   + 16;
-    float* vj   = ui   + BB*TT*NN;
-    float* xl2  = vj   + BB*TT*NN;
-    float* xr2  = xl2  + RWS;
-    float* hseq = xr2  + RWS;
-    float4* WT4 = (float4*)(hseq + BB*TT*HH);
-
-    k_mask <<<dim3(8,8,2), 256, 0, stream>>>(dynW, sadj, M0, M1, hseq, g1_att, g1_Wr, g1_Wl, AB,
-                                             Whh0, Wih1, Whh1, WT4);
-    k_gat1f<<<dim3(NN/4, BB*TT), 256, 0, stream>>>(x_seq, M0, M1, g1_Wl, g1_Wr, g1_att, g1_b, AB,
-                                                   g2_Wl, g2_Wr, g2_att, xl2, xr2, ui, vj);
-    k_gat2 <<<dim3(NN/32, BB*TT), 512, 0, stream>>>(xl2, xr2, M0, M1, g2_att, ui, vj, g2_b, hseq);
-    k_gru2 <<<1, 512, 0, stream>>>(hseq, Wih0, bih0, WT4, bhh0, Wih1, bih1, bhh1,
-                                   lamp, attnW, attnb, W1, b1, lng, lnb, W2, b2, out);
+    p.M0 = (uchar*)d_ws;
+    p.M1 = p.M0 + (size_t)NN*NN;
+    float* fb = (float*)(p.M1 + (size_t)NN*NN);
+    p.AB   = fb;
+    p.ui   = p.AB   + 16;
+    p.vj   = p.ui   + BB*TT*NN;
+    p.xl2  = p.vj   + BB*TT*NN;
+    p.xr2  = p.xl2  + RWS;
+    p.hseq = p.xr2  + RWS;
+    p.WT4  = (float4*)(p.hseq + BB*TT*HH);
+
+    void* args[] = { &p };
+    hipLaunchCooperativeKernel((const void*)k_fused, dim3(256), dim3(512),
+                               args, 0, stream);
 }
```

After: 333.1 us. 49.2% more time.
